# Kernel optimization log

Measured on AMD Instinct MI355X. Metric: run time of the kernel, lower is better.

## Reference

```python
import jax, jax.numpy as jnp
from jax import lax
import numpy as np

# Module hyperparameters (match init_kwargs)
N = 4            # number of multiplex cells per feature map
NUM_FM = 64      # feature maps in the input
NF = N * NUM_FM  # lateral channel count = 256
H = W = 32       # feature map height/width
D = 2            # lateral neighborhood radius
PRD = 2          # padding repair distance (must equal D for symmetric pad)
KS = 2 * D + 1   # lateral kernel size = 5
IOTA = 0.1       # blend of activation vs lateral support for winner selection
B = 16           # batch size


def minmax_fm(x):
    """Min-max normalize each feature map (over the last two dims) to [0,1].
    Degenerate (constant) maps map to 0."""
    mn = jnp.min(x, axis=(-2, -1), keepdims=True)
    mx = jnp.max(x, axis=(-2, -1), keepdims=True)
    denom = mx - mn
    safe = jnp.where(denom > 0, denom, 1.0)
    return jnp.where(denom > 0, (x - mn) / safe, 0.0)


def _pad(A):
    # pad_activations: zeros of shape (.., PRD+D+H, PRD+D+W), A at [PRD:-PRD]
    # with PRD == D this is symmetric (PRD, D) padding.
    return jnp.pad(A, ((0, 0), (0, 0), (PRD, D), (PRD, D)))


def _conv(x, w):
    # x: (B, Cin, H', W'), w: (Cout, Cin, KS, KS) -> VALID conv (padding=0)
    return lax.conv_general_dilated(x, w, (1, 1), 'VALID',
                                    dimension_numbers=('NCHW', 'OIHW', 'NCHW'))


def setup_inputs() -> dict:
    key = jax.random.key(0)
    k1, k2 = jax.random.split(key)
    A = jax.random.uniform(k1, (B, NUM_FM, H, W), dtype=jnp.float32)
    K = jax.random.normal(k2, (NF, NF, KS, KS), dtype=jnp.float32)  # trained lateral kernel
    S = jnp.ones((NF,), dtype=jnp.float32)                          # scaling param
    return {"A": A, "K": K, "S": S}


def reference(A, K, S):
    batch = A.shape[0]
    # A.repeat(1, n, 1, 1): tile input n times along channels -> (B, NF, H, W)
    A_rep = jnp.tile(A, (1, N, 1, 1))

    # First lateral pass: conv with minmax-normalized K^T, scaled by S, minmaxed.
    L1 = _conv(_pad(A_rep), minmax_fm(jnp.swapaxes(K, 0, 1))) / NUM_FM
    L1 = L1 * S[None, :, None, None]
    L1 = minmax_fm(L1)

    # Winner-take-all multiplex selection (deterministic branch):
    s = jnp.sum((1.0 - IOTA) * A_rep + IOTA * L1, axis=(-2, -1))  # (B, NF)
    s = jnp.swapaxes(s.reshape(batch, N, NUM_FM), 1, 2)            # (B, NUM_FM, N)
    A_max = jnp.argmax(s, axis=-1)                                  # (B, NUM_FM)
    fm_idx = NUM_FM * A_max + jnp.arange(NUM_FM)                    # (B, NUM_FM) channel ids

    # Active-channel mask (complement = inactive_multiplex_idx in the original)
    active = jnp.zeros((batch, NF), dtype=bool)
    active = active.at[jnp.arange(batch)[:, None], fm_idx].set(True)

    # Zero inactive channels of A (tmp_A) and diagonal K[i,i] for inactive i
    # (large_K[b, idx, idx] = 0 is pairwise/diagonal fancy indexing in torch).
    tmp_A = A_rep * active[:, :, None, None].astype(A_rep.dtype)
    eye = jnp.eye(NF, dtype=bool)
    kill = eye[None, :, :] & (~active)[:, :, None]                  # (B, NF, NF)
    large_K = jnp.where(kill[..., None, None], 0.0, K[None])        # (B, NF, NF, KS, KS)

    # Second lateral pass: per-sample conv with per-sample kernel.
    pA = _pad(tmp_A)

    def per_sample(x, Kb):
        w = minmax_fm(jnp.swapaxes(Kb, 0, 1))
        return _conv(x[None], w)[0]

    L2 = jax.vmap(per_sample)(pA, large_K) / NUM_FM                 # (B, NF, H, W)

    # Gather winning channels: filtered_L (B, NUM_FM, H, W)
    return jnp.take_along_axis(L2, fm_idx[:, :, None, None], axis=1)
```

## Files before the change

kernel.cpp:

```cpp
#include <hip/hip_runtime.h>


#define NFM 64
#define NMX 4
#define NFC 256
#define HW 1024
#define KK 25

typedef unsigned short u16;
typedef short short8 __attribute__((ext_vector_type(8)));
typedef float f32x4 __attribute__((ext_vector_type(4)));

__device__ __forceinline__ u16 f2bfbits(float f) {
    unsigned int u = __float_as_uint(f);
    u += 0x7fffu + ((u >> 16) & 1u);
    return (u16)(u >> 16);
}
__device__ __forceinline__ float bf2f(u16 v) {
    return __uint_as_float(((unsigned int)v) << 16);
}

__global__ __launch_bounds__(256) void kprep(const float* __restrict__ K,
                                             float* __restrict__ wsum2) {
    __shared__ __align__(16) float buf[64 * KK];
    int g = blockIdx.x & 63, o0 = (blockIdx.x >> 6) * 64;
    int t = threadIdx.x;
    float wacc[KK];
#pragma unroll
    for (int k = 0; k < KK; ++k) wacc[k] = 0.f;

    for (int n = 0; n < NMX; ++n) {
        int i = n * NFM + g;
        const float4* src = (const float4*)(K + (i * NFC + o0) * KK);
        __syncthreads();
        ((float4*)buf)[t] = src[t];
        if (t < 144) ((float4*)buf)[t + 256] = src[t + 256];
        __syncthreads();
        if (t < 64) {
            float v[KK];
            float mn = 1e30f, mx = -1e30f;
#pragma unroll
            for (int k = 0; k < KK; ++k) {
                v[k] = buf[t * KK + k];
                mn = fminf(mn, v[k]);
                mx = fmaxf(mx, v[k]);
            }
            float d = mx - mn;
            float r = d > 0.f ? 1.f / d : 0.f;
#pragma unroll
            for (int k = 0; k < KK; ++k) wacc[k] += (v[k] - mn) * r;
        }
    }
    __syncthreads();
    if (t < 64) {
#pragma unroll
        for (int k = 0; k < KK; ++k) buf[t * KK + k] = wacc[k];
    }
    __syncthreads();
    float4* dst = (float4*)(wsum2 + (g * NFC + o0) * KK);
    dst[t] = ((float4*)buf)[t];
    if (t < 144) dst[t + 256] = ((float4*)buf)[t + 256];
}

__global__ __launch_bounds__(256) void kpackW(const float* __restrict__ wsum2,
                                              char* __restrict__ Wpk) {
    int id = blockIdx.x * 256 + threadIdx.x;
    int o = id / 200;
    int rem = id - o * 200;
    int ks = rem >> 2, quad = rem & 3;
    int dydx = ks >> 1;
    int gb = (ks & 1) * 32 + quad * 8;
    short8 hs, ls;
#pragma unroll
    for (int j = 0; j < 8; ++j) {
        float v = wsum2[((gb + j) * NFC + o) * KK + dydx];
        u16 h = f2bfbits(v);
        float lo = v - bf2f(h);
        hs[j] = (short)h;
        ls[j] = (short)f2bfbits(lo);
    }
    char* base = Wpk + (((o >> 4) * 50 + ks) * 2048) + (quad * 16 + (o & 15)) * 16;
    *(short8*)(base) = hs;
    *(short8*)(base + 1024) = ls;
}

__global__ __launch_bounds__(256, 2) void kscore(const float* __restrict__ A,
                                                 const char* __restrict__ Wpk,
                                                 float4* __restrict__ part) {
    __shared__ u16 slabh[6 * 36 * 72];
    __shared__ u16 slabl[6 * 36 * 72];
    int t = threadIdx.x;
    int mh = blockIdx.x, yb2 = blockIdx.y, b = blockIdx.z;
    int y0 = yb2 * 2;
    int lane = t & 63;
    int wv = __builtin_amdgcn_readfirstlane(t >> 6);
    int n15 = lane & 15, quad = lane >> 4;

    const float* Ab = A + b * NFM * HW;
    for (int ry = 0; ry < 6; ++ry) {
        int gy = y0 - 2 + ry;
        bool rowok = (gy >= 0) && (gy < 32);
        for (int c = 0; c < 9; ++c) {
            int id2 = c * 256 + t;
            int g = (id2 * 3641) >> 17;
            int xi = id2 - g * 36;
            float v = 0.f;
            if (rowok && xi >= 2 && xi < 34)
                v = Ab[g * HW + gy * 32 + xi - 2];
            u16 h = f2bfbits(v);
            u16 l = f2bfbits(v - bf2f(h));
            int idx = (ry * 36 + xi) * 72 + g;
            slabh[idx] = h;
            slabl[idx] = l;
        }
    }
    __syncthreads();

    f32x4 acc[2][4];
#pragma unroll
    for (int m = 0; m < 2; ++m)
#pragma unroll
        for (int p = 0; p < 4; ++p)
#pragma unroll
            for (int r = 0; r < 4; ++r) acc[m][p][r] = 0.f;

    const char* wbase = Wpk + ((mh * 8 + wv * 2) * 50) * 2048 + lane * 16;

    for (int ks = 0; ks < 50; ++ks) {
        int dydx = ks >> 1;
        int gh = (ks & 1) * 32;
        int dy = dydx / 5, dx = dydx - dy * 5;
        short8 bh[4], bl[4];
#pragma unroll
        for (int p = 0; p < 4; ++p) {
            int r = p >> 1, nt = p & 1;
            int addr = ((r + dy) * 36 + nt * 16 + n15 + dx) * 72 + gh + quad * 8;
            bh[p] = *(const short8*)(slabh + addr);
            bl[p] = *(const short8*)(slabl + addr);
        }
#pragma unroll
        for (int m = 0; m < 2; ++m) {
            const char* cb = wbase + ((m * 50 + ks) << 11);
            short8 ah = *(const short8*)(cb);
            short8 al = *(const short8*)(cb + 1024);
#pragma unroll
            for (int p = 0; p < 4; ++p) {
                acc[m][p] = __builtin_amdgcn_mfma_f32_16x16x32_bf16(ah, bh[p], acc[m][p], 0, 0, 0);
                acc[m][p] = __builtin_amdgcn_mfma_f32_16x16x32_bf16(ah, bl[p], acc[m][p], 0, 0, 0);
                acc[m][p] = __builtin_amdgcn_mfma_f32_16x16x32_bf16(al, bh[p], acc[m][p], 0, 0, 0);
            }
        }
    }

#pragma unroll
    for (int m = 0; m < 2; ++m) {
#pragma unroll
        for (int reg = 0; reg < 4; ++reg) {
            float v0 = acc[m][0][reg], v1 = acc[m][1][reg];
            float v2 = acc[m][2][reg], v3 = acc[m][3][reg];
            float mn = fminf(fminf(v0, v1), fminf(v2, v3));
            float mx = fmaxf(fmaxf(v0, v1), fmaxf(v2, v3));
            float sm = (v0 + v1) + (v2 + v3);
#pragma unroll
            for (int msk = 1; msk <= 8; msk <<= 1) {
                mn = fminf(mn, __shfl_xor(mn, msk, 64));
                mx = fmaxf(mx, __shfl_xor(mx, msk, 64));
                sm += __shfl_xor(sm, msk, 64);
            }
            if (n15 == 0) {
                int o = mh * 128 + (wv * 2 + m) * 16 + quad * 4 + reg;
                part[(b * NFC + o) * 16 + yb2] = make_float4(mn, mx, sm, 0.f);
            }
        }
    }
}

__global__ __launch_bounds__(256) void kfin(const float4* __restrict__ part,
                                            const float* __restrict__ S,
                                            int* __restrict__ ig) {
    __shared__ float scl[NFC];
    int b = blockIdx.x, t = threadIdx.x;
    const float4* pp = part + (b * NFC + t) * 16;
    float mn = 1e30f, mx = -1e30f, sm = 0.f;
#pragma unroll
    for (int r = 0; r < 16; ++r) {
        float4 p = pp[r];
        mn = fminf(mn, p.x);
        mx = fmaxf(mx, p.y);
        sm += p.z;
    }
    float s = S[t] * (1.f / 64.f);
    float mnv = (s >= 0.f ? mn : mx) * s;
    float mxv = (s >= 0.f ? mx : mn) * s;
    float smv = sm * s;
    float d = mxv - mnv;
    scl[t] = d > 0.f ? (smv - 1024.f * mnv) / d : 0.f;
    __syncthreads();
    if (t < NFM) {
        float best = scl[t];
        int bi = 0;
#pragma unroll
        for (int n = 1; n < NMX; ++n) {
            float v = scl[n * NFM + t];
            if (v > best) { best = v; bi = n; }
        }
        ig[b * NFM + t] = bi * NFM + t;
    }
}

__global__ __launch_bounds__(256) void kpackO(const float* __restrict__ K,
                                              const int* __restrict__ ig,
                                              char* __restrict__ Wob) {
    __shared__ int igL[NFM];
    int b = blockIdx.x >> 4, fq = blockIdx.x & 15;
    int t = threadIdx.x;
    if (t < NFM) igL[t] = ig[b * NFM + t];
    __syncthreads();
    int fl = t >> 6, g = t & 63;
    int f = fq * 4 + fl;
    int o = igL[f], i = igL[g];
    const float* src = K + (i * NFC + o) * KK;
    float v[KK];
    float mn = 1e30f, mx = -1e30f;
#pragma unroll
    for (int k = 0; k < KK; ++k) {
        v[k] = src[k];
        mn = fminf(mn, v[k]);
        mx = fmaxf(mx, v[k]);
    }
    float d = mx - mn;
    float r = d > 0.f ? 1.f / d : 0.f;
    int gh = g >> 5;
    char* base = Wob + b * 409600 + (f >> 4) * 50 * 2048
               + ((((g & 31) >> 3) * 16 + (f & 15)) * 16) + (g & 7) * 2;
#pragma unroll
    for (int k = 0; k < KK; ++k) {
        float nv = (v[k] - mn) * r;
        u16 h = f2bfbits(nv);
        u16 l = f2bfbits(nv - bf2f(h));
        char* p = base + (2 * k + gh) * 2048;
        *(u16*)p = h;
        *(u16*)(p + 1024) = l;
    }
}

__global__ __launch_bounds__(256, 2) void kout(const float* __restrict__ A,
                                               const char* __restrict__ Wob,
                                               float* __restrict__ out) {
    __shared__ u16 slabh[6 * 20 * 72];
    __shared__ u16 slabl[6 * 20 * 72];
    int t = threadIdx.x;
    int xh = blockIdx.x, yb2 = blockIdx.y, b = blockIdx.z;
    int y0 = yb2 * 2, x0 = xh * 16;
    int lane = t & 63;
    int wv = __builtin_amdgcn_readfirstlane(t >> 6);
    int n15 = lane & 15, quad = lane >> 4;

    const float* Ab = A + b * NFM * HW;
    for (int ry = 0; ry < 6; ++ry) {
        int gy = y0 - 2 + ry;
        bool rowok = (gy >= 0) && (gy < 32);
        for (int c = 0; c < 5; ++c) {
            int id2 = c * 256 + t;
            int g = (id2 * 6554) >> 17;
            int xi = id2 - g * 20;
            int x = x0 + xi - 2;
            float v = 0.f;
            if (rowok && x >= 0 && x < 32)
                v = Ab[g * HW + gy * 32 + x];
            u16 h = f2bfbits(v);
            u16 l = f2bfbits(v - bf2f(h));
            int idx = (ry * 20 + xi) * 72 + g;
            slabh[idx] = h;
            slabl[idx] = l;
        }
    }
    __syncthreads();

    f32x4 acc[2];
#pragma unroll
    for (int r = 0; r < 2; ++r)
#pragma unroll
        for (int j = 0; j < 4; ++j) acc[r][j] = 0.f;

    const char* wbase = Wob + b * 409600 + (wv * 50) * 2048 + lane * 16;

    for (int ks = 0; ks < 50; ++ks) {
        int dydx = ks >> 1;
        int gh = (ks & 1) * 32;
        int dy = dydx / 5, dx = dydx - dy * 5;
        const char* cb = wbase + (ks << 11);
        short8 ah = *(const short8*)(cb);
        short8 al = *(const short8*)(cb + 1024);
#pragma unroll
        for (int r = 0; r < 2; ++r) {
            int addr = ((r + dy) * 20 + n15 + dx) * 72 + gh + quad * 8;
            short8 bh = *(const short8*)(slabh + addr);
            short8 bl = *(const short8*)(slabl + addr);
            acc[r] = __builtin_amdgcn_mfma_f32_16x16x32_bf16(ah, bh, acc[r], 0, 0, 0);
            acc[r] = __builtin_amdgcn_mfma_f32_16x16x32_bf16(ah, bl, acc[r], 0, 0, 0);
            acc[r] = __builtin_amdgcn_mfma_f32_16x16x32_bf16(al, bh, acc[r], 0, 0, 0);
        }
    }

#pragma unroll
    for (int r = 0; r < 2; ++r)
#pragma unroll
        for (int reg = 0; reg < 4; ++reg) {
            int f = wv * 16 + quad * 4 + reg;
            out[(b * NFM + f) * HW + (y0 + r) * 32 + x0 + n15] = acc[r][reg] * (1.f / 64.f);
        }
}

extern "C" void kernel_launch(void* const* d_in, const int* in_sizes, int n_in,
                              void* d_out, int out_size, void* d_ws, size_t ws_size,
                              hipStream_t stream) {
    const float* A = (const float*)d_in[0];
    const float* K = (const float*)d_in[1];
    const float* S = (const float*)d_in[2];
    float* out = (float*)d_out;

    char* ws = (char*)d_ws;
    char*   Wpk   = ws;
    float*  wsum2 = (float*)(ws + 1638400);
    float4* part  = (float4*)(ws + 3276800);
    char*   Wob   = ws + 1638400;
    int*    igv   = (int*)(ws + 8192000);

    kprep<<<dim3(256), dim3(256), 0, stream>>>(K, wsum2);
    kpackW<<<dim3(200), dim3(256), 0, stream>>>(wsum2, Wpk);
    kscore<<<dim3(2, 16, 16), dim3(256), 0, stream>>>(A, Wpk, part);
    kfin<<<dim3(16), dim3(256), 0, stream>>>(part, S, igv);
    kpackO<<<dim3(256), dim3(256), 0, stream>>>(K, igv, Wob);
    kout<<<dim3(2, 16, 16), dim3(256), 0, stream>>>(A, Wob, out);
}
```

Baseline: 154.6 us.

## Split kscore across 8 waves, prefetch weights, stage kpackO writes in LDS

kscore now runs 512 threads with one 16-row output tile per wave instead of two, which halves per-wave accumulators so more waves can overlap. kscore and kout prefetch the next step's weight fragment from global memory to hide load latency, and kout's launch bounds ask for higher occupancy. kpackO builds each output tile in shared memory and then writes it to global with coalesced float4 stores instead of scattered 2-byte writes. In exchange, each kscore block loads its A slab once for 8 waves, and the larger kscore block size adds register and scheduling pressure.

```diff
diff --git a/kernel.cpp b/kernel.cpp
--- a/kernel.cpp
+++ b/kernel.cpp
@@ -84,7 +84,7 @@
     *(short8*)(base + 1024) = ls;
 }
 
-__global__ __launch_bounds__(256, 2) void kscore(const float* __restrict__ A,
+__global__ __launch_bounds__(512, 4) void kscore(const float* __restrict__ A,
                                                  const char* __restrict__ Wpk,
                                                  float4* __restrict__ part) {
     __shared__ u16 slabh[6 * 36 * 72];
@@ -100,33 +100,40 @@
     for (int ry = 0; ry < 6; ++ry) {
         int gy = y0 - 2 + ry;
         bool rowok = (gy >= 0) && (gy < 32);
-        for (int c = 0; c < 9; ++c) {
-            int id2 = c * 256 + t;
-            int g = (id2 * 3641) >> 17;
-            int xi = id2 - g * 36;
-            float v = 0.f;
-            if (rowok && xi >= 2 && xi < 34)
-                v = Ab[g * HW + gy * 32 + xi - 2];
-            u16 h = f2bfbits(v);
-            u16 l = f2bfbits(v - bf2f(h));
-            int idx = (ry * 36 + xi) * 72 + g;
-            slabh[idx] = h;
-            slabl[idx] = l;
-        }
-    }
-    __syncthreads();
-
-    f32x4 acc[2][4];
-#pragma unroll
-    for (int m = 0; m < 2; ++m)
-#pragma unroll
-        for (int p = 0; p < 4; ++p)
-#pragma unroll
-            for (int r = 0; r < 4; ++r) acc[m][p][r] = 0.f;
-
-    const char* wbase = Wpk + ((mh * 8 + wv * 2) * 50) * 2048 + lane * 16;
+        for (int c = 0; c < 5; ++c) {
+            int id2 = c * 512 + t;
+            if (id2 < 2304) {
+                int g = (id2 * 3641) >> 17;
+                int xi = id2 - g * 36;
+                float v = 0.f;
+                if (rowok && xi >= 2 && xi < 34)
+                    v = Ab[g * HW + gy * 32 + xi - 2];
+                u16 h = f2bfbits(v);
+                u16 l = f2bfbits(v - bf2f(h));
+                int idx = (ry * 36 + xi) * 72 + g;
+                slabh[idx] = h;
+                slabl[idx] = l;
+            }
+        }
+    }
+    __syncthreads();
+
+    f32x4 acc[4];
+#pragma unroll
+    for (int p = 0; p < 4; ++p)
+#pragma unroll
+        for (int r = 0; r < 4; ++r) acc[p][r] = 0.f;
+
+    const char* wbase = Wpk + ((mh * 8 + wv) * 50) * 2048 + lane * 16;
+    short8 cah = *(const short8*)(wbase);
+    short8 cal = *(const short8*)(wbase + 1024);
 
     for (int ks = 0; ks < 50; ++ks) {
+        int ksn = ks < 49 ? ks + 1 : 49;
+        const char* nb = wbase + (ksn << 11);
+        short8 nah = *(const short8*)nb;
+        short8 nal = *(const short8*)(nb + 1024);
+
         int dydx = ks >> 1;
         int gh = (ks & 1) * 32;
         int dy = dydx / 5, dx = dydx - dy * 5;
@@ -139,38 +146,31 @@
             bl[p] = *(const short8*)(slabl + addr);
         }
 #pragma unroll
-        for (int m = 0; m < 2; ++m) {
-            const char* cb = wbase + ((m * 50 + ks) << 11);
-            short8 ah = *(const short8*)(cb);
-            short8 al = *(const short8*)(cb + 1024);
-#pragma unroll
-            for (int p = 0; p < 4; ++p) {
-                acc[m][p] = __builtin_amdgcn_mfma_f32_16x16x32_bf16(ah, bh[p], acc[m][p], 0, 0, 0);
-                acc[m][p] = __builtin_amdgcn_mfma_f32_16x16x32_bf16(ah, bl[p], acc[m][p], 0, 0, 0);
-                acc[m][p] = __builtin_amdgcn_mfma_f32_16x16x32_bf16(al, bh[p], acc[m][p], 0, 0, 0);
-            }
-        }
-    }
-
-#pragma unroll
-    for (int m = 0; m < 2; ++m) {
-#pragma unroll
-        for (int reg = 0; reg < 4; ++reg) {
-            float v0 = acc[m][0][reg], v1 = acc[m][1][reg];
-            float v2 = acc[m][2][reg], v3 = acc[m][3][reg];
-            float mn = fminf(fminf(v0, v1), fminf(v2, v3));
-            float mx = fmaxf(fmaxf(v0, v1), fmaxf(v2, v3));
-            float sm = (v0 + v1) + (v2 + v3);
-#pragma unroll
-            for (int msk = 1; msk <= 8; msk <<= 1) {
-                mn = fminf(mn, __shfl_xor(mn, msk, 64));
-                mx = fmaxf(mx, __shfl_xor(mx, msk, 64));
-                sm += __shfl_xor(sm, msk, 64);
-            }
-            if (n15 == 0) {
-                int o = mh * 128 + (wv * 2 + m) * 16 + quad * 4 + reg;
-                part[(b * NFC + o) * 16 + yb2] = make_float4(mn, mx, sm, 0.f);
-            }
+        for (int p = 0; p < 4; ++p) {
+            acc[p] = __builtin_amdgcn_mfma_f32_16x16x32_bf16(cah, bh[p], acc[p], 0, 0, 0);
+            acc[p] = __builtin_amdgcn_mfma_f32_16x16x32_bf16(cah, bl[p], acc[p], 0, 0, 0);
+            acc[p] = __builtin_amdgcn_mfma_f32_16x16x32_bf16(cal, bh[p], acc[p], 0, 0, 0);
+        }
+        cah = nah;
+        cal = nal;
+    }
+
+#pragma unroll
+    for (int reg = 0; reg < 4; ++reg) {
+        float v0 = acc[0][reg], v1 = acc[1][reg];
+        float v2 = acc[2][reg], v3 = acc[3][reg];
+        float mn = fminf(fminf(v0, v1), fminf(v2, v3));
+        float mx = fmaxf(fmaxf(v0, v1), fmaxf(v2, v3));
+        float sm = (v0 + v1) + (v2 + v3);
+#pragma unroll
+        for (int msk = 1; msk <= 8; msk <<= 1) {
+            mn = fminf(mn, __shfl_xor(mn, msk, 64));
+            mx = fmaxf(mx, __shfl_xor(mx, msk, 64));
+            sm += __shfl_xor(sm, msk, 64);
+        }
+        if (n15 == 0) {
+            int o = (mh * 8 + wv) * 16 + quad * 4 + reg;
+            part[(b * NFC + o) * 16 + yb2] = make_float4(mn, mx, sm, 0.f);
         }
     }
 }
@@ -212,39 +212,53 @@
                                               const int* __restrict__ ig,
                                               char* __restrict__ Wob) {
     __shared__ int igL[NFM];
-    int b = blockIdx.x >> 4, fq = blockIdx.x & 15;
+    __shared__ __align__(16) char cbuf[25 * 2048];
+    int ft = blockIdx.x, b = blockIdx.y;
     int t = threadIdx.x;
     if (t < NFM) igL[t] = ig[b * NFM + t];
     __syncthreads();
-    int fl = t >> 6, g = t & 63;
-    int f = fq * 4 + fl;
-    int o = igL[f], i = igL[g];
-    const float* src = K + (i * NFC + o) * KK;
-    float v[KK];
-    float mn = 1e30f, mx = -1e30f;
-#pragma unroll
-    for (int k = 0; k < KK; ++k) {
-        v[k] = src[k];
-        mn = fminf(mn, v[k]);
-        mx = fmaxf(mx, v[k]);
-    }
-    float d = mx - mn;
-    float r = d > 0.f ? 1.f / d : 0.f;
-    int gh = g >> 5;
-    char* base = Wob + b * 409600 + (f >> 4) * 50 * 2048
-               + ((((g & 31) >> 3) * 16 + (f & 15)) * 16) + (g & 7) * 2;
-#pragma unroll
-    for (int k = 0; k < KK; ++k) {
-        float nv = (v[k] - mn) * r;
-        u16 h = f2bfbits(nv);
-        u16 l = f2bfbits(nv - bf2f(h));
-        char* p = base + (2 * k + gh) * 2048;
-        *(u16*)p = h;
-        *(u16*)(p + 1024) = l;
-    }
-}
-
-__global__ __launch_bounds__(256, 2) void kout(const float* __restrict__ A,
+    int g32 = t & 31, fh = t >> 5;
+    int quad = g32 >> 3, j = g32 & 7;
+    char* wdst = Wob + b * 409600 + ft * 102400;
+
+    for (int half = 0; half < 2; ++half) {
+        int i = igL[half * 32 + g32];
+#pragma unroll
+        for (int e = 0; e < 2; ++e) {
+            int f15 = fh * 2 + e;
+            int o = igL[ft * 16 + f15];
+            const float* src = K + (i * NFC + o) * KK;
+            float v[KK];
+            float mn = 1e30f, mx = -1e30f;
+#pragma unroll
+            for (int k = 0; k < KK; ++k) {
+                v[k] = src[k];
+                mn = fminf(mn, v[k]);
+                mx = fmaxf(mx, v[k]);
+            }
+            float d = mx - mn;
+            float r = d > 0.f ? 1.f / d : 0.f;
+            char* base = cbuf + (quad * 16 + f15) * 16 + j * 2;
+#pragma unroll
+            for (int k = 0; k < KK; ++k) {
+                float nv = (v[k] - mn) * r;
+                u16 h = f2bfbits(nv);
+                u16 l = f2bfbits(nv - bf2f(h));
+                *(u16*)(base + k * 2048) = h;
+                *(u16*)(base + k * 2048 + 1024) = l;
+            }
+        }
+        __syncthreads();
+        for (int idx = t; idx < 3200; idx += 256) {
+            int ch = idx >> 7, w = idx & 127;
+            *(float4*)(wdst + (ch * 2 + half) * 2048 + w * 16) =
+                *(const float4*)(cbuf + ch * 2048 + w * 16);
+        }
+        __syncthreads();
+    }
+}
+
+__global__ __launch_bounds__(256, 4) void kout(const float* __restrict__ A,
                                                const char* __restrict__ Wob,
                                                float* __restrict__ out) {
     __shared__ u16 slabh[6 * 20 * 72];
@@ -281,26 +295,32 @@
 #pragma unroll
     for (int r = 0; r < 2; ++r)
 #pragma unroll
-        for (int j = 0; j < 4; ++j) acc[r][j] = 0.f;
+        for (int jr = 0; jr < 4; ++jr) acc[r][jr] = 0.f;
 
     const char* wbase = Wob + b * 409600 + (wv * 50) * 2048 + lane * 16;
+    short8 cah = *(const short8*)(wbase);
+    short8 cal = *(const short8*)(wbase + 1024);
 
     for (int ks = 0; ks < 50; ++ks) {
+        int ksn = ks < 49 ? ks + 1 : 49;
+        const char* nb = wbase + (ksn << 11);
+        short8 nah = *(const short8*)nb;
+        short8 nal = *(const short8*)(nb + 1024);
+
         int dydx = ks >> 1;
         int gh = (ks & 1) * 32;
         int dy = dydx / 5, dx = dydx - dy * 5;
-        const char* cb = wbase + (ks << 11);
-        short8 ah = *(const short8*)(cb);
-        short8 al = *(const short8*)(cb + 1024);
 #pragma unroll
         for (int r = 0; r < 2; ++r) {
             int addr = ((r + dy) * 20 + n15 + dx) * 72 + gh + quad * 8;
             short8 bh = *(const short8*)(slabh + addr);
             short8 bl = *(const short8*)(slabl + addr);
-            acc[r] = __builtin_amdgcn_mfma_f32_16x16x32_bf16(ah, bh, acc[r], 0, 0, 0);
-            acc[r] = __builtin_amdgcn_mfma_f32_16x16x32_bf16(ah, bl, acc[r], 0, 0, 0);
-            acc[r] = __builtin_amdgcn_mfma_f32_16x16x32_bf16(al, bh, acc[r], 0, 0, 0);
-        }
+            acc[r] = __builtin_amdgcn_mfma_f32_16x16x32_bf16(cah, bh, acc[r], 0, 0, 0);
+            acc[r] = __builtin_amdgcn_mfma_f32_16x16x32_bf16(cah, bl, acc[r], 0, 0, 0);
+            acc[r] = __builtin_amdgcn_mfma_f32_16x16x32_bf16(cal, bh, acc[r], 0, 0, 0);
+        }
+        cah = nah;
+        cal = nal;
     }
 
 #pragma unroll
@@ -329,8 +349,8 @@
 
     kprep<<<dim3(256), dim3(256), 0, stream>>>(K, wsum2);
     kpackW<<<dim3(200), dim3(256), 0, stream>>>(wsum2, Wpk);
-    kscore<<<dim3(2, 16, 16), dim3(256), 0, stream>>>(A, Wpk, part);
+    kscore<<<dim3(2, 16, 16), dim3(512), 0, stream>>>(A, Wpk, part);
     kfin<<<dim3(16), dim3(256), 0, stream>>>(part, S, igv);
-    kpackO<<<dim3(256), dim3(256), 0, stream>>>(K, igv, Wob);
+    kpackO<<<dim3(4, 16), dim3(256), 0, stream>>>(K, igv, Wob);
     kout<<<dim3(2, 16, 16), dim3(256), 0, stream>>>(A, Wob, out);
 }
```

Measured after the change: 154.8 us. About the same (+0.1%).
